# Optimization experiments

Hardware: AMD Instinct MI355X
Metric: run time of the kernel (lower is better)

Reference implementation:

```python
import jax, jax.numpy as jnp
import numpy as np

HEAD = 16

def setup_inputs() -> dict:
    key = jax.random.key(0)
    k1, k2, k3 = jax.random.split(key, 3)
    B, S, D = 2, 2048, 1024
    x = jax.random.normal(k1, (B, S, D), dtype=jnp.float32)
    w_qkv = jax.random.normal(k2, (D, 3 * D), dtype=jnp.float32) * (1.0 / np.sqrt(D))
    b_qkv = jnp.zeros((3 * D,), dtype=jnp.float32)
    w_out = jax.random.normal(k3, (D, D), dtype=jnp.float32) * (1.0 / np.sqrt(D))
    b_out = jnp.zeros((D,), dtype=jnp.float32)
    return {"x": x, "w_qkv": w_qkv, "b_qkv": b_qkv, "w_out": w_out, "b_out": b_out}


def reference(x, w_qkv, b_qkv, w_out, b_out):
    B, S, D = x.shape
    hd = D // HEAD  # head dim
    qkv = x @ w_qkv + b_qkv                      # [B,S,3D]
    qkv = qkv.reshape(B, S, 3, HEAD, hd)
    qkv = jnp.transpose(qkv, (2, 0, 3, 1, 4))    # [3,B,H,S,hd]
    q, k, v = qkv[0], qkv[1], qkv[2]
    scores = jnp.einsum('bhqd,bhkd->bhqk', q, k)  # [B,H,S,S]
    causal = jnp.triu(jnp.ones((S, S), dtype=bool), k=1)
    scores = jnp.where(causal, -jnp.inf, scores)
    scores = scores / jnp.sqrt(jnp.asarray(hd, dtype=x.dtype))
    attn = jax.nn.softmax(scores, axis=-1)
    z = jnp.einsum('bhqk,bhkd->bhqd', attn, v)   # [B,H,S,hd]
    z = jnp.transpose(z, (0, 2, 1, 3)).reshape(B, S, D)
    out = z @ w_out + b_out
    return out
```

## Files before the change

### kernel.cpp

```cpp
#include <hip/hip_runtime.h>

#define S_LEN  2048
#define NH     16
#define HD     64
#define DMODEL 1024

using bf16x8 = __attribute__((ext_vector_type(8))) __bf16;
using f32x4  = __attribute__((ext_vector_type(4))) float;

__device__ __forceinline__ unsigned short f2bf(float f) {
    unsigned u = __float_as_uint(f);
    u += 0x7FFFu + ((u >> 16) & 1u);
    return (unsigned short)(u >> 16);
}
__device__ __forceinline__ unsigned pk_trunc(float lo, float hi) {
    return __builtin_amdgcn_perm(__float_as_uint(hi), __float_as_uint(lo), 0x07060302u);
}

#define EXP2(x) __builtin_amdgcn_exp2f(x)

#define GLDS16(gsrc, ldst) \
    __builtin_amdgcn_global_load_lds((__attribute__((address_space(1))) void*)(gsrc), \
                                     (__attribute__((address_space(3))) void*)(ldst), 16, 0, 0)

#define WAIT_LGKM0() __builtin_amdgcn_s_waitcnt(0xC07F)

#define ASM_VMCNT(n)  asm volatile("s_waitcnt vmcnt(" #n ")" ::: "memory")
#define ASM_BARRIER() asm volatile("s_barrier" ::: "memory")

__global__ __launch_bounds__(256) void prep_kernel(
    const float* __restrict__ x, const float* __restrict__ w_qkv,
    const float* __restrict__ w_out,
    unsigned short* __restrict__ xb, unsigned short* __restrict__ wqkvT,
    unsigned short* __restrict__ woutT) {
    __shared__ float T[32][33];
    int bx = blockIdx.x;
    if (bx < 4096) {
        int idx = (bx * 256 + threadIdx.x) * 4;
        float4 v = *(const float4*)(x + idx);
        ushort4 o;
        o.x = f2bf(v.x); o.y = f2bf(v.y); o.z = f2bf(v.z); o.w = f2bf(v.w);
        *(ushort4*)(xb + idx) = o;
        return;
    }
    int tb = bx - 4096;
    int tcol = tb & 127, krow = tb >> 7;
    const float* in;
    unsigned short* out;
    int N, nbx;
    if (tcol < 96) { in = w_qkv; out = wqkvT; N = 3072; nbx = tcol; }
    else           { in = w_out; out = woutT; N = 1024; nbx = tcol - 96; }
    int r  = threadIdx.x >> 3;
    int c4 = (threadIdx.x & 7) * 4;
    int kbase = krow * 32, nbase = nbx * 32;
    float4 v = *(const float4*)(in + (size_t)(kbase + r) * N + nbase + c4);
    T[r][c4 + 0] = v.x; T[r][c4 + 1] = v.y; T[r][c4 + 2] = v.z; T[r][c4 + 3] = v.w;
    __syncthreads();
    ushort4 o;
    o.x = f2bf(T[c4 + 0][r]); o.y = f2bf(T[c4 + 1][r]);
    o.z = f2bf(T[c4 + 2][r]); o.w = f2bf(T[c4 + 3][r]);
    *(ushort4*)(out + (size_t)(nbase + r) * 1024 + kbase + c4) = o;
}

template <int NI, int NT>
__device__ __forceinline__ void mfma_mainloop64(const unsigned short* __restrict__ A,
                                                const unsigned short* __restrict__ B,
                                                int m0, int n0,
                                                unsigned short* As, unsigned short* Bs,
                                                f32x4 acc[4][NI]) {
    constexpr int K = NT * 64;
    const int lane = threadIdx.x & 63, wave = threadIdx.x >> 6;
    const int quad = lane >> 4, l15 = lane & 15;
    const int wm0 = (wave >> 1) * 64, wn0 = (wave & 1) * (NI * 16);

    auto stageA = [&](int t) {
        unsigned short* Ad = As + (t % 3) * 8192;
        #pragma unroll
        for (int j = 0; j < 4; ++j) {
            int c0 = j * 256 + wave * 64;
            int c  = c0 + lane;
            int r = c >> 3, pc = c & 7, q = pc ^ (r & 7);
            GLDS16(A + (size_t)(m0 + r) * K + t * 64 + q * 8, Ad + c0 * 8);
        }
    };
    auto stageB = [&](int t) {
        unsigned short* Bd = Bs + (t & 1) * (NI * 2048);
        #pragma unroll
        for (int j = 0; j < NI; ++j) {
            int c0 = j * 256 + wave * 64;
            int c  = c0 + lane;
            int r = c >> 3, pc = c & 7, q = pc ^ (r & 7);
            GLDS16(B + (size_t)(n0 + r) * K + t * 64 + q * 8, Bd + c0 * 8);
        }
    };

    stageB(0); stageA(0);
    stageB(1); stageA(1);
    stageA(2);

    #pragma unroll
    for (int t = 0; t < NT; ++t) {
        if (t < NT - 1) { ASM_VMCNT(4); } else { ASM_VMCNT(0); }
        ASM_BARRIER();
        if (t >= 1) {
            if (t + 1 < NT) stageB(t + 1);
            if (t + 2 < NT) stageA(t + 2);
        }

        const unsigned short* Ab = As + (t % 3) * 8192;
        const unsigned short* Bb = Bs + (t & 1) * (NI * 2048);
        bf16x8 af[2][4], bfr[2][NI];
        #pragma unroll
        for (int mi = 0; mi < 4; ++mi) {
            int r = wm0 + mi * 16 + l15, x = r & 7;
            af[0][mi] = *(const bf16x8*)(Ab + r * 64 + ((quad    ) ^ x) * 8);
            af[1][mi] = *(const bf16x8*)(Ab + r * 64 + ((4 + quad) ^ x) * 8);
        }
        #pragma unroll
        for (int ni = 0; ni < NI; ++ni) {
            int r = wn0 + ni * 16 + l15, x = r & 7;
            bfr[0][ni] = *(const bf16x8*)(Bb + r * 64 + ((quad    ) ^ x) * 8);
            bfr[1][ni] = *(const bf16x8*)(Bb + r * 64 + ((4 + quad) ^ x) * 8);
        }
        #pragma unroll
        for (int h = 0; h < 2; ++h)
            #pragma unroll
            for (int mi = 0; mi < 4; ++mi)
                #pragma unroll
                for (int ni = 0; ni < NI; ++ni)
                    acc[mi][ni] = __builtin_amdgcn_mfma_f32_16x16x32_bf16(
                        af[h][mi], bfr[h][ni], acc[mi][ni], 0, 0, 0);
    }
}

__global__ __launch_bounds__(256) void gemm_qkv_kernel(
    const unsigned short* __restrict__ xb, const unsigned short* __restrict__ wT,
    const float* __restrict__ bias,
    unsigned short* __restrict__ Qt, unsigned short* __restrict__ Kh,
    unsigned short* __restrict__ Vt) {
    __shared__ __align__(16) unsigned short Sh[40960];
    unsigned short* As = Sh;
    unsigned short* Bs = Sh + 24576;

    f32x4 acc[4][4];
    #pragma unroll
    for (int i = 0; i < 4; ++i)
        #pragma unroll
        for (int j = 0; j < 4; ++j) acc[i][j] = (f32x4){0.f, 0.f, 0.f, 0.f};

    const int bid = blockIdx.x;
    const int xcd = bid & 7, slot = bid >> 3;
    const int nt = xcd * 3 + (slot % 3);
    const int mt = slot / 3;
    const int m0 = mt * 128, n0 = nt * 128;
    mfma_mainloop64<4, 16>(xb, wT, m0, n0, As, Bs, acc);

    const int lane = threadIdx.x & 63, wave = threadIdx.x >> 6;
    const int quad = lane >> 4, l15 = lane & 15;
    const int wm0 = (wave >> 1) * 64, wn0 = (wave & 1) * 64;

    const int colbase = n0 + wn0;
    const int t = colbase >> 10;
    const int h = (colbase >> 6) & (NH - 1);
    const float qscale = (t == 0) ? 0.125f * 1.44269504088896f : 1.0f;
    float bv[4];
    #pragma unroll
    for (int ni = 0; ni < 4; ++ni) bv[ni] = bias[colbase + ni * 16 + l15];

    __syncthreads();
    unsigned short* Lw = Sh + wave * 1536;

    #pragma unroll
    for (int mi = 0; mi < 4; ++mi) {
        int mbase = m0 + wm0 + mi * 16;
        int b = mbase >> 11, sbase = mbase & (S_LEN - 1);
        if (t == 1) {
            #pragma unroll
            for (int ni = 0; ni < 4; ++ni)
                #pragma unroll
                for (int r = 0; r < 4; ++r)
                    Lw[(quad * 4 + r) * 72 + ni * 16 + l15] =
                        f2bf(acc[mi][ni][r] + bv[ni]);
            WAIT_LGKM0();
            int rr = lane & 15, dc = (lane >> 4) * 16;
            uint4 v0 = *(const uint4*)(Lw + rr * 72 + dc);
            uint4 v1 = *(const uint4*)(Lw + rr * 72 + dc + 8);
            unsigned short* dst =
                Kh + ((size_t)(b * NH + h) * S_LEN + sbase + rr) * HD + dc;
            *(uint4*)dst = v0;
            *(uint4*)(dst + 8) = v1;
        } else {
            #pragma unroll
            for (int ni = 0; ni < 4; ++ni)
                #pragma unroll
                for (int r = 0; r < 4; ++r)
                    Lw[(ni * 16 + l15) * 24 + quad * 4 + r] =
                        f2bf((acc[mi][ni][r] + bv[ni]) * qscale);
            WAIT_LGKM0();
            int c = lane;
            uint4 v0 = *(const uint4*)(Lw + c * 24);
            uint4 v1 = *(const uint4*)(Lw + c * 24 + 8);
            unsigned short* base = (t == 0) ? Qt : Vt;
            unsigned short* dst =
                base + ((size_t)(b * NH + h) * HD + c) * S_LEN + sbase;
            *(uint4*)dst = v0;
            *(uint4*)(dst + 8) = v1;
        }
        WAIT_LGKM0();
    }
}

__global__ __launch_bounds__(256) void gemm_out_kernel(
    const unsigned short* __restrict__ zb, const unsigned short* __restrict__ wT,
    const float* __restrict__ bias, float* __restrict__ out) {
    __shared__ __align__(16) unsigned short As[24576], Bs[8192];
    f32x4 acc[4][2];
    #pragma unroll
    for (int i = 0; i < 4; ++i)
        #pragma unroll
        for (int j = 0; j < 2; ++j) acc[i][j] = (f32x4){0.f, 0.f, 0.f, 0.f};

    const int bid = blockIdx.x;
    const int xcd = bid & 7, slot = bid >> 3;
    const int nt = xcd * 2 + (slot & 1);
    const int mt = slot >> 1;
    const int m0 = mt * 128, n0 = nt * 64;
    mfma_mainloop64<2, 16>(zb, wT, m0, n0, As, Bs, acc);

    const int lane = threadIdx.x & 63, wave = threadIdx.x >> 6;
    const int quad = lane >> 4, l15 = lane & 15;
    const int wm0 = (wave >> 1) * 64, wn0 = (wave & 1) * 32;
    #pragma unroll
    for (int mi = 0; mi < 4; ++mi) {
        #pragma unroll
        for (int ni = 0; ni < 2; ++ni) {
            int col = n0 + wn0 + ni * 16 + l15;
            float bvv = bias[col];
            #pragma unroll
            for (int r = 0; r < 4; ++r)
                out[(size_t)(m0 + wm0 + mi * 16 + quad * 4 + r) * DMODEL + col] =
                    acc[mi][ni][r] + bvv;
        }
    }
}

__device__ const int g_sched[15 * 4] = {
    5,0,11,6,   5,12,23,7,  2,0,11,-1,
    7,0,10,0,   7,11,21,1,  7,22,31,2,
    6,0,9,3,    4,0,9,8,    4,10,19,9,
    6,10,18,4,  6,19,27,5,
    3,0,7,10,   3,8,15,11,  1,0,7,-1,  0,0,3,-1
};

__global__ __launch_bounds__(1024, 8) void attn_mfma_kernel(
    const unsigned short* __restrict__ Qt, const unsigned short* __restrict__ Kh,
    const unsigned short* __restrict__ Vt, unsigned short* __restrict__ zb,
    float* __restrict__ Zp, float* __restrict__ lp) {
    __shared__ __align__(16) unsigned short Ks[2 * 64 * 64];
    __shared__ __align__(16) unsigned short Vs[2 * 64 * 64];
    __shared__ __align__(16) unsigned short Pl[16 * 16 * 64];

    const int lane = threadIdx.x & 63, wave = threadIdx.x >> 6;
    const int quad = lane >> 4, l15 = lane & 15;
    const int bh = blockIdx.x;
    const int qt   = g_sched[blockIdx.y * 4 + 0];
    const int klo  = g_sched[blockIdx.y * 4 + 1];
    const int khi  = g_sched[blockIdx.y * 4 + 2];
    const int part = g_sched[blockIdx.y * 4 + 3];
    const int q0 = qt * 256;
    const float M0 = 12.0f;

    bf16x8 qf0, qf1;
    {
        const unsigned short* qb = Qt + (size_t)bh * HD * S_LEN + q0 + wave * 16 + l15;
        union { bf16x8 v; unsigned short u[8]; } u0, u1;
        #pragma unroll
        for (int j = 0; j < 8; ++j) {
            u0.u[j] = qb[(quad * 8 + j) * S_LEN];
            u1.u[j] = qb[(32 + quad * 8 + j) * S_LEN];
        }
        qf0 = u0.v; qf1 = u1.v;
    }
    bf16x8 onesv;
    {
        union { bf16x8 v; unsigned short u[8]; } uo;
        #pragma unroll
        for (int j = 0; j < 8; ++j) uo.u[j] = 0x3F80;
        onesv = uo.v;
    }

    f32x4 Z[4];
    #pragma unroll
    for (int i = 0; i < 4; ++i) Z[i] = (f32x4){0.f, 0.f, 0.f, 0.f};
    f32x4 racc = (f32x4){0.f, 0.f, 0.f, 0.f};

    unsigned short* pw = Pl + wave * 1024;
    const int pwrow = l15 * 64;

    auto stageKV = [&](int kt, int b) {
        if (wave < 8) {
            int c0 = wave * 64;
            int c  = c0 + lane;
            int r = c >> 3, pc = c & 7, q = pc ^ (r & 7);
            GLDS16(Kh + ((size_t)bh * S_LEN + kt * 64 + r) * HD + q * 8,
                   Ks + b * 4096 + c0 * 8);
        } else {
            int c0 = (wave - 8) * 64;
            int c  = c0 + lane;
            int d = c >> 3, pc = c & 7, q = pc ^ (d & 7);
            GLDS16(Vt + ((size_t)bh * HD + d) * S_LEN + kt * 64 + q * 8,
                   Vs + b * 4096 + c0 * 8);
        }
    };

    auto body = [&](int kt, int cb, bool pref) {
        if (pref) {
            stageKV(kt + 1, cb ^ 1);
            ASM_VMCNT(1);
        } else {
            ASM_VMCNT(0);
        }
        ASM_BARRIER();

        const unsigned short* Kb = Ks + cb * 4096;
        const unsigned short* Vb = Vs + cb * 4096;

        const int kq = kt - 4 * qt;
        const int dw = wave - (kq << 2);

        if (kq < 0 || dw >= 4) {
            #pragma unroll
            for (int n = 0; n < 4; ++n) {
                int woff = pwrow + (((2 * n + (quad >> 1)) ^ (l15 & 7)) << 3) + (quad & 1) * 4;
                int rk = n * 16 + l15;
                int x = rk & 7;
                bf16x8 kv0 = *(const bf16x8*)(Kb + rk * 64 + ((quad    ) ^ x) * 8);
                bf16x8 kv1 = *(const bf16x8*)(Kb + rk * 64 + ((4 + quad) ^ x) * 8);
                f32x4 t4 = (f32x4){-M0, -M0, -M0, -M0};
                __builtin_amdgcn_s_setprio(1);
                t4 = __builtin_amdgcn_mfma_f32_16x16x32_bf16(kv0, qf0, t4, 0, 0, 0);
                t4 = __builtin_amdgcn_mfma_f32_16x16x32_bf16(kv1, qf1, t4, 0, 0, 0);
                __builtin_amdgcn_s_setprio(0);
                uint2 pk;
                pk.x = pk_trunc(EXP2(t4[0]), EXP2(t4[1]));
                pk.y = pk_trunc(EXP2(t4[2]), EXP2(t4[3]));
                *(uint2*)(pw + woff) = pk;
            }
            #pragma unroll
            for (int kh = 0; kh < 2; ++kh) {
                bf16x8 pa = *(const bf16x8*)(pw + pwrow + ((kh * 4 + quad) ^ (l15 & 7)) * 8);
                __builtin_amdgcn_s_setprio(1);
                racc = __builtin_amdgcn_mfma_f32_16x16x32_bf16(onesv, pa, racc, 0, 0, 0);
                #pragma unroll
                for (int ni = 0; ni < 4; ++ni) {
                    int rd = ni * 16 + l15;
                    bf16x8 vb = *(const bf16x8*)(Vb + rd * 64 + ((kh * 4 + quad) ^ (rd & 7)) * 8);
                    Z[ni] = __builtin_amdgcn_mfma_f32_16x16x32_bf16(vb, pa, Z[ni], 0, 0, 0);
                }
                __builtin_amdgcn_s_setprio(0);
            }
        } else if (dw >= 0) {
            const int nmax = dw;
            const int qthr = dw * 16 + l15 - quad * 4;
            #pragma unroll
            for (int n = 0; n < 4; ++n) {
                int woff = pwrow + (((2 * n + (quad >> 1)) ^ (l15 & 7)) << 3) + (quad & 1) * 4;
                if (n <= nmax) {
                    int rk = n * 16 + l15;
                    int x = rk & 7;
                    bf16x8 kv0 = *(const bf16x8*)(Kb + rk * 64 + ((quad    ) ^ x) * 8);
                    bf16x8 kv1 = *(const bf16x8*)(Kb + rk * 64 + ((4 + quad) ^ x) * 8);
                    f32x4 t4 = (f32x4){-M0, -M0, -M0, -M0};
                    __builtin_amdgcn_s_setprio(1);
                    t4 = __builtin_amdgcn_mfma_f32_16x16x32_bf16(kv0, qf0, t4, 0, 0, 0);
                    t4 = __builtin_amdgcn_mfma_f32_16x16x32_bf16(kv1, qf1, t4, 0, 0, 0);
                    __builtin_amdgcn_s_setprio(0);
                    float p[4];
                    #pragma unroll
                    for (int r = 0; r < 4; ++r) {
                        p[r] = EXP2(t4[r]);
                        if ((n * 16 + r) > qthr) p[r] = 0.f;
                    }
                    uint2 pk;
                    pk.x = pk_trunc(p[0], p[1]);
                    pk.y = pk_trunc(p[2], p[3]);
                    *(uint2*)(pw + woff) = pk;
                } else {
                    *(uint2*)(pw + woff) = (uint2){0u, 0u};
                }
            }
            const int khmax = dw >> 1;
            for (int kh = 0; kh <= khmax; ++kh) {
                bf16x8 pa = *(const bf16x8*)(pw + pwrow + ((kh * 4 + quad) ^ (l15 & 7)) * 8);
                __builtin_amdgcn_s_setprio(1);
                racc = __builtin_amdgcn_mfma_f32_16x16x32_bf16(onesv, pa, racc, 0, 0, 0);
                #pragma unroll
                for (int ni = 0; ni < 4; ++ni) {
                    int rd = ni * 16 + l15;
                    bf16x8 vb = *(const bf16x8*)(Vb + rd * 64 + ((kh * 4 + quad) ^ (rd & 7)) * 8);
                    Z[ni] = __builtin_amdgcn_mfma_f32_16x16x32_bf16(vb, pa, Z[ni], 0, 0, 0);
                }
                __builtin_amdgcn_s_setprio(0);
            }
        }
        ASM_BARRIER();
    };

    stageKV(klo, 0);
    {
        int cnt = khi - klo + 1;
        int kt = klo;
        while (cnt >= 2) {
            body(kt, 0, true);
            body(kt + 1, 1, cnt > 2);
            kt += 2; cnt -= 2;
        }
        if (cnt == 1) body(kt, 0, false);
    }

    const float rsum = racc[0];

    const int ql = wave * 16 + l15;
    if (part < 0) {
        const int b = bh >> 4, h = bh & (NH - 1);
        float inv = 1.f / rsum;
        size_t rowoff = (size_t)(b * S_LEN + q0 + ql) * DMODEL + h * HD;
        #pragma unroll
        for (int ni = 0; ni < 4; ++ni) {
            ushort4 o;
            o.x = f2bf(Z[ni][0] * inv);
            o.y = f2bf(Z[ni][1] * inv);
            o.z = f2bf(Z[ni][2] * inv);
            o.w = f2bf(Z[ni][3] * inv);
            *(ushort4*)(zb + rowoff + ni * 16 + quad * 4) = o;
        }
    } else {
        float* zpo = Zp + ((size_t)(part * 32 + bh) * 256 + ql) * 64;
        #pragma unroll
        for (int ni = 0; ni < 4; ++ni) {
            float4 st;
            st.x = Z[ni][0]; st.y = Z[ni][1]; st.z = Z[ni][2]; st.w = Z[ni][3];
            *(float4*)(zpo + ni * 16 + quad * 4) = st;
        }
        if (quad == 0)
            lp[(size_t)(part * 32 + bh) * 256 + ql] = rsum;
    }
}

__global__ __launch_bounds__(256) void attn_merge_kernel(
    const float* __restrict__ Zp, const float* __restrict__ lp,
    unsigned short* __restrict__ zb) {
    const int qt_tab[5] = {7, 6, 5, 4, 3};
    const int s0_tab[5] = {0, 3, 6, 8, 10};
    const int np_tab[5] = {3, 3, 2, 2, 2};
    const int bh = blockIdx.x, y = blockIdx.y;
    const int qt = qt_tab[y], s0 = s0_tab[y], np = np_tab[y];
    const int t = threadIdx.x;
    const int b = bh >> 4, h = bh & (NH - 1);
    #pragma unroll
    for (int chunk = 0; chunk < 4; ++chunk) {
        const int q  = chunk * 64 + (t >> 2);
        const int d0 = (t & 3) << 4;
        float l = 0.f;
        for (int p = 0; p < np; ++p)
            l += lp[(size_t)((s0 + p) * 32 + bh) * 256 + q];
        float inv = 1.f / l;
        unsigned short* o =
            zb + (size_t)(b * S_LEN + qt * 256 + q) * DMODEL + h * HD + d0;
        #pragma unroll
        for (int i = 0; i < 16; i += 4) {
            float4 s = {0.f, 0.f, 0.f, 0.f};
            for (int p = 0; p < np; ++p) {
                const float* zp = Zp + ((size_t)((s0 + p) * 32 + bh) * 256 + q) * 64 + d0 + i;
                float4 a = *(const float4*)zp;
                s.x += a.x; s.y += a.y; s.z += a.z; s.w += a.w;
            }
            ushort4 ov;
            ov.x = f2bf(s.x * inv);
            ov.y = f2bf(s.y * inv);
            ov.z = f2bf(s.z * inv);
            ov.w = f2bf(s.w * inv);
            *(ushort4*)(o + i) = ov;
        }
    }
}

extern "C" void kernel_launch(void* const* d_in, const int* in_sizes, int n_in,
                              void* d_out, int out_size, void* d_ws, size_t ws_size,
                              hipStream_t stream)
{
    const float* x     = (const float*)d_in[0];
    const float* w_qkv = (const float*)d_in[1];
    const float* b_qkv = (const float*)d_in[2];
    const float* w_out = (const float*)d_in[3];
    const float* b_out = (const float*)d_in[4];
    float* out = (float*)d_out;

    unsigned short* wsu   = (unsigned short*)d_ws;
    unsigned short* xb    = wsu;
    unsigned short* wqkvT = xb    + (size_t)4194304;
    unsigned short* woutT = wqkvT + (size_t)3145728;
    unsigned short* Qt    = woutT + (size_t)1048576;
    unsigned short* Kh    = Qt    + (size_t)4194304;
    unsigned short* Vt    = Kh    + (size_t)4194304;
    unsigned short* zb    = Vt    + (size_t)4194304;
    float* Zp = (float*)(zb + (size_t)4194304);
    float* lp = Zp + (size_t)12 * 32 * 256 * 64;

    prep_kernel<<<dim3(8192), 256, 0, stream>>>(x, w_qkv, w_out, xb, wqkvT, woutT);

    gemm_qkv_kernel<<<dim3(768), 256, 0, stream>>>(
        xb, wqkvT, b_qkv, Qt, Kh, Vt);

    attn_mfma_kernel<<<dim3(2 * NH, 15), 1024, 0, stream>>>(Qt, Kh, Vt, zb, Zp, lp);
    attn_merge_kernel<<<dim3(2 * NH, 5), 256, 0, stream>>>(Zp, lp, zb);

    gemm_out_kernel<<<dim3(512), 256, 0, stream>>>(
        zb, woutT, b_out, out);
}
```

Baseline: 193.2 us.

## Process two 16-row query groups per wave in attention kernel, halving block size

Each wave now handles 32 query rows (two 16-row groups) instead of 16, so the attention block shrinks from 16 waves to 8. Every K and V fragment read from LDS now feeds two MFMAs, which cuts LDS read traffic per unit of work. Each wave stages both a K and a V chunk per tile, with the vmcnt wait raised to match. The cost is roughly double the accumulator and Q registers per wave, fewer waves to hide latency, and per-group causal masking logic on the diagonal tiles.

```diff
diff --git a/kernel.cpp b/kernel.cpp
--- a/kernel.cpp
+++ b/kernel.cpp
@@ -252,13 +252,13 @@
     3,0,7,10,   3,8,15,11,  1,0,7,-1,  0,0,3,-1
 };
 
-__global__ __launch_bounds__(1024, 8) void attn_mfma_kernel(
+__global__ __launch_bounds__(512, 4) void attn_mfma_kernel(
     const unsigned short* __restrict__ Qt, const unsigned short* __restrict__ Kh,
     const unsigned short* __restrict__ Vt, unsigned short* __restrict__ zb,
     float* __restrict__ Zp, float* __restrict__ lp) {
     __shared__ __align__(16) unsigned short Ks[2 * 64 * 64];
     __shared__ __align__(16) unsigned short Vs[2 * 64 * 64];
-    __shared__ __align__(16) unsigned short Pl[16 * 16 * 64];
+    __shared__ __align__(16) unsigned short Pl[8 * 2048];
 
     const int lane = threadIdx.x & 63, wave = threadIdx.x >> 6;
     const int quad = lane >> 4, l15 = lane & 15;
@@ -270,16 +270,18 @@
     const int q0 = qt * 256;
     const float M0 = 12.0f;
 
-    bf16x8 qf0, qf1;
-    {
-        const unsigned short* qb = Qt + (size_t)bh * HD * S_LEN + q0 + wave * 16 + l15;
+    bf16x8 qf[2][2];
+    #pragma unroll
+    for (int g = 0; g < 2; ++g) {
+        const unsigned short* qb =
+            Qt + (size_t)bh * HD * S_LEN + q0 + wave * 32 + g * 16 + l15;
         union { bf16x8 v; unsigned short u[8]; } u0, u1;
         #pragma unroll
         for (int j = 0; j < 8; ++j) {
             u0.u[j] = qb[(quad * 8 + j) * S_LEN];
             u1.u[j] = qb[(32 + quad * 8 + j) * S_LEN];
         }
-        qf0 = u0.v; qf1 = u1.v;
+        qf[g][0] = u0.v; qf[g][1] = u1.v;
     }
     bf16x8 onesv;
     {
@@ -289,23 +291,28 @@
         onesv = uo.v;
     }
 
-    f32x4 Z[4];
-    #pragma unroll
-    for (int i = 0; i < 4; ++i) Z[i] = (f32x4){0.f, 0.f, 0.f, 0.f};
-    f32x4 racc = (f32x4){0.f, 0.f, 0.f, 0.f};
-
-    unsigned short* pw = Pl + wave * 1024;
+    f32x4 Z[2][4];
+    #pragma unroll
+    for (int g = 0; g < 2; ++g)
+        #pragma unroll
+        for (int i = 0; i < 4; ++i) Z[g][i] = (f32x4){0.f, 0.f, 0.f, 0.f};
+    f32x4 racc[2];
+    racc[0] = (f32x4){0.f, 0.f, 0.f, 0.f};
+    racc[1] = (f32x4){0.f, 0.f, 0.f, 0.f};
+
+    unsigned short* pw = Pl + wave * 2048;
     const int pwrow = l15 * 64;
 
     auto stageKV = [&](int kt, int b) {
-        if (wave < 8) {
+        {
             int c0 = wave * 64;
             int c  = c0 + lane;
             int r = c >> 3, pc = c & 7, q = pc ^ (r & 7);
             GLDS16(Kh + ((size_t)bh * S_LEN + kt * 64 + r) * HD + q * 8,
                    Ks + b * 4096 + c0 * 8);
-        } else {
-            int c0 = (wave - 8) * 64;
+        }
+        {
+            int c0 = wave * 64;
             int c  = c0 + lane;
             int d = c >> 3, pc = c & 7, q = pc ^ (d & 7);
             GLDS16(Vt + ((size_t)bh * HD + d) * S_LEN + kt * 64 + q * 8,
@@ -316,7 +323,7 @@
     auto body = [&](int kt, int cb, bool pref) {
         if (pref) {
             stageKV(kt + 1, cb ^ 1);
-            ASM_VMCNT(1);
+            ASM_VMCNT(2);
         } else {
             ASM_VMCNT(0);
         }
@@ -326,81 +333,98 @@
         const unsigned short* Vb = Vs + cb * 4096;
 
         const int kq = kt - 4 * qt;
-        const int dw = wave - (kq << 2);
-
-        if (kq < 0 || dw >= 4) {
+        const int dwg0 = 2 * wave - (kq << 2);
+
+        if (kq < 0 || dwg0 >= 4) {
             #pragma unroll
             for (int n = 0; n < 4; ++n) {
-                int woff = pwrow + (((2 * n + (quad >> 1)) ^ (l15 & 7)) << 3) + (quad & 1) * 4;
+                int wsw = (((2 * n + (quad >> 1)) ^ (l15 & 7)) << 3) + (quad & 1) * 4;
                 int rk = n * 16 + l15;
                 int x = rk & 7;
                 bf16x8 kv0 = *(const bf16x8*)(Kb + rk * 64 + ((quad    ) ^ x) * 8);
                 bf16x8 kv1 = *(const bf16x8*)(Kb + rk * 64 + ((4 + quad) ^ x) * 8);
-                f32x4 t4 = (f32x4){-M0, -M0, -M0, -M0};
+                f32x4 t4a = (f32x4){-M0, -M0, -M0, -M0};
+                f32x4 t4b = (f32x4){-M0, -M0, -M0, -M0};
                 __builtin_amdgcn_s_setprio(1);
-                t4 = __builtin_amdgcn_mfma_f32_16x16x32_bf16(kv0, qf0, t4, 0, 0, 0);
-                t4 = __builtin_amdgcn_mfma_f32_16x16x32_bf16(kv1, qf1, t4, 0, 0, 0);
+                t4a = __builtin_amdgcn_mfma_f32_16x16x32_bf16(kv0, qf[0][0], t4a, 0, 0, 0);
+                t4a = __builtin_amdgcn_mfma_f32_16x16x32_bf16(kv1, qf[0][1], t4a, 0, 0, 0);
+                t4b = __builtin_amdgcn_mfma_f32_16x16x32_bf16(kv0, qf[1][0], t4b, 0, 0, 0);
+                t4b = __builtin_amdgcn_mfma_f32_16x16x32_bf16(kv1, qf[1][1], t4b, 0, 0, 0);
                 __builtin_amdgcn_s_setprio(0);
-                uint2 pk;
-                pk.x = pk_trunc(EXP2(t4[0]), EXP2(t4[1]));
-                pk.y = pk_trunc(EXP2(t4[2]), EXP2(t4[3]));
-                *(uint2*)(pw + woff) = pk;
+                uint2 pka, pkb;
+                pka.x = pk_trunc(EXP2(t4a[0]), EXP2(t4a[1]));
+                pka.y = pk_trunc(EXP2(t4a[2]), EXP2(t4a[3]));
+                pkb.x = pk_trunc(EXP2(t4b[0]), EXP2(t4b[1]));
+                pkb.y = pk_trunc(EXP2(t4b[2]), EXP2(t4b[3]));
+                *(uint2*)(pw + pwrow + wsw)        = pka;
+                *(uint2*)(pw + 1024 + pwrow + wsw) = pkb;
             }
             #pragma unroll
             for (int kh = 0; kh < 2; ++kh) {
-                bf16x8 pa = *(const bf16x8*)(pw + pwrow + ((kh * 4 + quad) ^ (l15 & 7)) * 8);
+                int psw = ((kh * 4 + quad) ^ (l15 & 7)) * 8;
+                bf16x8 pa0 = *(const bf16x8*)(pw + pwrow + psw);
+                bf16x8 pa1 = *(const bf16x8*)(pw + 1024 + pwrow + psw);
                 __builtin_amdgcn_s_setprio(1);
-                racc = __builtin_amdgcn_mfma_f32_16x16x32_bf16(onesv, pa, racc, 0, 0, 0);
+                racc[0] = __builtin_amdgcn_mfma_f32_16x16x32_bf16(onesv, pa0, racc[0], 0, 0, 0);
+                racc[1] = __builtin_amdgcn_mfma_f32_16x16x32_bf16(onesv, pa1, racc[1], 0, 0, 0);
                 #pragma unroll
                 for (int ni = 0; ni < 4; ++ni) {
                     int rd = ni * 16 + l15;
                     bf16x8 vb = *(const bf16x8*)(Vb + rd * 64 + ((kh * 4 + quad) ^ (rd & 7)) * 8);
-                    Z[ni] = __builtin_amdgcn_mfma_f32_16x16x32_bf16(vb, pa, Z[ni], 0, 0, 0);
+                    Z[0][ni] = __builtin_amdgcn_mfma_f32_16x16x32_bf16(vb, pa0, Z[0][ni], 0, 0, 0);
+                    Z[1][ni] = __builtin_amdgcn_mfma_f32_16x16x32_bf16(vb, pa1, Z[1][ni], 0, 0, 0);
                 }
                 __builtin_amdgcn_s_setprio(0);
             }
-        } else if (dw >= 0) {
-            const int nmax = dw;
-            const int qthr = dw * 16 + l15 - quad * 4;
-            #pragma unroll
-            for (int n = 0; n < 4; ++n) {
-                int woff = pwrow + (((2 * n + (quad >> 1)) ^ (l15 & 7)) << 3) + (quad & 1) * 4;
-                if (n <= nmax) {
-                    int rk = n * 16 + l15;
-                    int x = rk & 7;
-                    bf16x8 kv0 = *(const bf16x8*)(Kb + rk * 64 + ((quad    ) ^ x) * 8);
-                    bf16x8 kv1 = *(const bf16x8*)(Kb + rk * 64 + ((4 + quad) ^ x) * 8);
-                    f32x4 t4 = (f32x4){-M0, -M0, -M0, -M0};
+        } else if (dwg0 >= -1) {
+            #pragma unroll
+            for (int g = 0; g < 2; ++g) {
+                const int dwg = dwg0 + g;
+                if (dwg < 0) continue;
+                const int nmax = dwg < 3 ? dwg : 3;
+                const int qthr = dwg * 16 + l15 - quad * 4;
+                #pragma unroll
+                for (int n = 0; n < 4; ++n) {
+                    int woff = g * 1024 + pwrow +
+                               (((2 * n + (quad >> 1)) ^ (l15 & 7)) << 3) + (quad & 1) * 4;
+                    if (n <= nmax) {
+                        int rk = n * 16 + l15;
+                        int x = rk & 7;
+                        bf16x8 kv0 = *(const bf16x8*)(Kb + rk * 64 + ((quad    ) ^ x) * 8);
+                        bf16x8 kv1 = *(const bf16x8*)(Kb + rk * 64 + ((4 + quad) ^ x) * 8);
+                        f32x4 t4 = (f32x4){-M0, -M0, -M0, -M0};
+                        __builtin_amdgcn_s_setprio(1);
+                        t4 = __builtin_amdgcn_mfma_f32_16x16x32_bf16(kv0, qf[g][0], t4, 0, 0, 0);
+                        t4 = __builtin_amdgcn_mfma_f32_16x16x32_bf16(kv1, qf[g][1], t4, 0, 0, 0);
+                        __builtin_amdgcn_s_setprio(0);
+                        float p[4];
+                        #pragma unroll
+                        for (int r = 0; r < 4; ++r) {
+                            p[r] = EXP2(t4[r]);
+                            if ((n * 16 + r) > qthr) p[r] = 0.f;
+                        }
+                        uint2 pk;
+                        pk.x = pk_trunc(p[0], p[1]);
+                        pk.y = pk_trunc(p[2], p[3]);
+                        *(uint2*)(pw + woff) = pk;
+                    } else {
+                        *(uint2*)(pw + woff) = (uint2){0u, 0u};
+                    }
+                }
+                const int khmax = (dwg >> 1) < 1 ? (dwg >> 1) : 1;
+                for (int kh = 0; kh <= khmax; ++kh) {
+                    int psw = ((kh * 4 + quad) ^ (l15 & 7)) * 8;
+                    bf16x8 pa = *(const bf16x8*)(pw + g * 1024 + pwrow + psw);
                     __builtin_amdgcn_s_setprio(1);
-                    t4 = __builtin_amdgcn_mfma_f32_16x16x32_bf16(kv0, qf0, t4, 0, 0, 0);
-                    t4 = __builtin_amdgcn_mfma_f32_16x16x32_bf16(kv1, qf1, t4, 0, 0, 0);
+                    racc[g] = __builtin_amdgcn_mfma_f32_16x16x32_bf16(onesv, pa, racc[g], 0, 0, 0);
+                    #pragma unroll
+                    for (int ni = 0; ni < 4; ++ni) {
+                        int rd = ni * 16 + l15;
+                        bf16x8 vb = *(const bf16x8*)(Vb + rd * 64 + ((kh * 4 + quad) ^ (rd & 7)) * 8);
+                        Z[g][ni] = __builtin_amdgcn_mfma_f32_16x16x32_bf16(vb, pa, Z[g][ni], 0, 0, 0);
+                    }
                     __builtin_amdgcn_s_setprio(0);
-                    float p[4];
-                    #pragma unroll
-                    for (int r = 0; r < 4; ++r) {
-                        p[r] = EXP2(t4[r]);
-                        if ((n * 16 + r) > qthr) p[r] = 0.f;
-                    }
-                    uint2 pk;
-                    pk.x = pk_trunc(p[0], p[1]);
-                    pk.y = pk_trunc(p[2], p[3]);
-                    *(uint2*)(pw + woff) = pk;
-                } else {
-                    *(uint2*)(pw + woff) = (uint2){0u, 0u};
                 }
-            }
-            const int khmax = dw >> 1;
-            for (int kh = 0; kh <= khmax; ++kh) {
-                bf16x8 pa = *(const bf16x8*)(pw + pwrow + ((kh * 4 + quad) ^ (l15 & 7)) * 8);
-                __builtin_amdgcn_s_setprio(1);
-                racc = __builtin_amdgcn_mfma_f32_16x16x32_bf16(onesv, pa, racc, 0, 0, 0);
-                #pragma unroll
-                for (int ni = 0; ni < 4; ++ni) {
-                    int rd = ni * 16 + l15;
-                    bf16x8 vb = *(const bf16x8*)(Vb + rd * 64 + ((kh * 4 + quad) ^ (rd & 7)) * 8);
-                    Z[ni] = __builtin_amdgcn_mfma_f32_16x16x32_bf16(vb, pa, Z[ni], 0, 0, 0);
-                }
-                __builtin_amdgcn_s_setprio(0);
             }
         }
         ASM_BARRIER();
@@ -418,32 +442,35 @@
         if (cnt == 1) body(kt, 0, false);
     }
 
-    const float rsum = racc[0];
-
-    const int ql = wave * 16 + l15;
-    if (part < 0) {
-        const int b = bh >> 4, h = bh & (NH - 1);
-        float inv = 1.f / rsum;
-        size_t rowoff = (size_t)(b * S_LEN + q0 + ql) * DMODEL + h * HD;
-        #pragma unroll
-        for (int ni = 0; ni < 4; ++ni) {
-            ushort4 o;
-            o.x = f2bf(Z[ni][0] * inv);
-            o.y = f2bf(Z[ni][1] * inv);
-            o.z = f2bf(Z[ni][2] * inv);
-            o.w = f2bf(Z[ni][3] * inv);
-            *(ushort4*)(zb + rowoff + ni * 16 + quad * 4) = o;
-        }
-    } else {
-        float* zpo = Zp + ((size_t)(part * 32 + bh) * 256 + ql) * 64;
-        #pragma unroll
-        for (int ni = 0; ni < 4; ++ni) {
-            float4 st;
-            st.x = Z[ni][0]; st.y = Z[ni][1]; st.z = Z[ni][2]; st.w = Z[ni][3];
-            *(float4*)(zpo + ni * 16 + quad * 4) = st;
-        }
-        if (quad == 0)
-            lp[(size_t)(part * 32 + bh) * 256 + ql] = rsum;
+    #pragma unroll
+    for (int g = 0; g < 2; ++g) {
+        const float rsum = racc[g][0];
+        const int ql = wave * 32 + g * 16 + l15;
+        if (part < 0) {
+            const int b = bh >> 4, h = bh & (NH - 1);
+            float inv = 1.f / rsum;
+            size_t rowoff = (size_t)(b * S_LEN + q0 + ql) * DMODEL + h * HD;
+            #pragma unroll
+            for (int ni = 0; ni < 4; ++ni) {
+                ushort4 o;
+                o.x = f2bf(Z[g][ni][0] * inv);
+                o.y = f2bf(Z[g][ni][1] * inv);
+                o.z = f2bf(Z[g][ni][2] * inv);
+                o.w = f2bf(Z[g][ni][3] * inv);
+                *(ushort4*)(zb + rowoff + ni * 16 + quad * 4) = o;
+            }
+        } else {
+            float* zpo = Zp + ((size_t)(part * 32 + bh) * 256 + ql) * 64;
+            #pragma unroll
+            for (int ni = 0; ni < 4; ++ni) {
+                float4 st;
+                st.x = Z[g][ni][0]; st.y = Z[g][ni][1];
+                st.z = Z[g][ni][2]; st.w = Z[g][ni][3];
+                *(float4*)(zpo + ni * 16 + quad * 4) = st;
+            }
+            if (quad == 0)
+                lp[(size_t)(part * 32 + bh) * 256 + ql] = rsum;
+        }
     }
 }
 
@@ -512,7 +539,7 @@
     gemm_qkv_kernel<<<dim3(768), 256, 0, stream>>>(
         xb, wqkvT, b_qkv, Qt, Kh, Vt);
 
-    attn_mfma_kernel<<<dim3(2 * NH, 15), 1024, 0, stream>>>(Qt, Kh, Vt, zb, Zp, lp);
+    attn_mfma_kernel<<<dim3(2 * NH, 15), 512, 0, stream>>>(Qt, Kh, Vt, zb, Zp, lp);
     attn_merge_kernel<<<dim3(2 * NH, 5), 256, 0, stream>>>(Zp, lp, zb);
 
     gemm_out_kernel<<<dim3(512), 256, 0, stream>>>(
```

After: 193.2 us. About the same (-0.0%).
